# Optimization experiments

Hardware: AMD Instinct MI355X
Metric: run time of the kernel (lower is better)

The kernel has to match this reference:

```python
import jax, jax.numpy as jnp
import numpy as np

D = 128          # hidden_channels
NU = 50000       # num user nodes
NI = 50000       # num item nodes
E = 600000       # edges per edge type
SLOPE = 0.01     # F.leaky_relu default negative_slope


def setup_inputs() -> dict:
    key = jax.random.key(0)
    ks = jax.random.split(key, 24)
    ws = 1.0 / np.sqrt(D)  # xavier-ish scale

    def W2(i):  # stacked [n_layers=2, D, D] weight
        return jax.random.normal(ks[i], (2, D, D), jnp.float32) * ws

    def B2(i):  # stacked [2, D] bias
        return jax.random.normal(ks[i], (2, D), jnp.float32) * 0.01

    inp = {
        "x_user": jax.random.normal(ks[0], (NU, D), jnp.float32),
        "x_item": jax.random.normal(ks[1], (NI, D), jnp.float32),
        # row 0 = src indices, row 1 = dst indices
        "ei_ui": jax.random.randint(ks[2], (2, E), 0, NU),  # user -> item (dst in [0,NI))
        "ei_iu": jax.random.randint(ks[3], (2, E), 0, NI),  # item -> user (dst in [0,NU))
        # per-node-type q/k/v Linear params, stacked over the 2 layers
        "q_w_user": W2(4),  "q_b_user": B2(5),
        "k_w_user": W2(6),  "k_b_user": B2(7),
        "v_w_user": W2(8),  "v_b_user": B2(9),
        "q_w_item": W2(10), "q_b_item": B2(11),
        "k_w_item": W2(12), "k_b_item": B2(13),
        "v_w_item": W2(14), "v_b_item": B2(15),
        # per-edge-type bilinear W, stacked over the 2 layers
        "W_ui": W2(16),
        "W_iu": W2(17),
    }
    return inp


def _edge_agg(x_src, x_dst, qw, qb, kw, kb, vw, vb, W, src, dst, n_dst):
    # torch Linear: x @ w.T + b
    q = x_src @ qw.T + qb            # [Nsrc, D]
    k = x_dst @ kw.T + kb            # [Ndst, D]
    v = x_src @ vw.T + vb            # [Nsrc, D]
    qW = q @ W                       # project on nodes (cheaper than per-edge)
    # per-edge bilinear score q_src . W . k_dst / sqrt(D)
    score = jnp.sum(qW[src] * k[dst], axis=-1) * (1.0 / np.sqrt(D))  # [E]
    alpha = jax.nn.softmax(jax.nn.leaky_relu(score, SLOPE))          # softmax over edges
    msg = alpha[:, None] * v[src]                                    # [E, D]
    return jax.ops.segment_sum(msg, dst, num_segments=n_dst)


def _layer(x_u, x_i, ei_ui, ei_iu, p, l):
    # edge type (user, rates, item): q/v from src type (user), k from dst type (item)
    agg_i = _edge_agg(x_u, x_i,
                      p["q_w_user"][l], p["q_b_user"][l],
                      p["k_w_item"][l], p["k_b_item"][l],
                      p["v_w_user"][l], p["v_b_user"][l],
                      p["W_ui"][l], ei_ui[0], ei_ui[1], NI)
    # edge type (item, rev_rates, user)
    agg_u = _edge_agg(x_i, x_u,
                      p["q_w_item"][l], p["q_b_item"][l],
                      p["k_w_user"][l], p["k_b_user"][l],
                      p["v_w_item"][l], p["v_b_item"][l],
                      p["W_iu"][l], ei_iu[0], ei_iu[1], NU)
    # out_dict initialized with x_dst.clone(), then scatter_add
    return x_u + agg_u, x_i + agg_i


def reference(x_user, x_item, ei_ui, ei_iu,
              q_w_user, q_b_user, k_w_user, k_b_user, v_w_user, v_b_user,
              q_w_item, q_b_item, k_w_item, k_b_item, v_w_item, v_b_item,
              W_ui, W_iu):
    p = dict(q_w_user=q_w_user, q_b_user=q_b_user, k_w_user=k_w_user,
             k_b_user=k_b_user, v_w_user=v_w_user, v_b_user=v_b_user,
             q_w_item=q_w_item, q_b_item=q_b_item, k_w_item=k_w_item,
             k_b_item=k_b_item, v_w_item=v_w_item, v_b_item=v_b_item,
             W_ui=W_ui, W_iu=W_iu)
    x_u, x_i = _layer(x_user, x_item, ei_ui, ei_iu, p, 0)  # conv1
    x_u, x_i = _layer(x_u, x_i, ei_ui, ei_iu, p, 1)        # conv2
    return jnp.concatenate([x_u, x_i], axis=0)  # [NU+NI, D]
```

## Files before the change

kernel.cpp:

```cpp
#include <hip/hip_runtime.h>
#include <stdint.h>

#define D 128

typedef __attribute__((ext_vector_type(8))) short bf16x8;
typedef __attribute__((ext_vector_type(4))) float f32x4;
typedef __attribute__((ext_vector_type(2))) float f32x2;
typedef unsigned short u16;
typedef unsigned char u8;
typedef unsigned int u32;

#define KSCALE (0.08838834764831845f * 1.4426950408889634f)

#if defined(__has_builtin)
#if __has_builtin(__builtin_amdgcn_cvt_pk_f32_fp8) && __has_builtin(__builtin_amdgcn_cvt_pk_fp8_f32)
#define HW_FP8 1
#endif
#if __has_builtin(__builtin_elementwise_fma)
#define VFMA(a, b, c) __builtin_elementwise_fma(a, b, c)
#else
#define VFMA(a, b, c) ((a) * (b) + (c))
#endif
#else
#define VFMA(a, b, c) ((a) * (b) + (c))
#endif

static __device__ __forceinline__ float b2f(u16 u) {
  return __uint_as_float(((unsigned)u) << 16);
}
static __device__ __forceinline__ u16 f2b(float f) {
  unsigned u = __float_as_uint(f);
  return (u16)((u + 0x7fffu + ((u >> 16) & 1u)) >> 16);
}

static __device__ __forceinline__ u8 enc_fp8(float f) {
#ifdef HW_FP8
  int p = __builtin_amdgcn_cvt_pk_fp8_f32(f, 0.f, 0, false);
  return (u8)(p & 0xff);
#else
  float a = fabsf(f);
  unsigned s = (__float_as_uint(f) >> 31) << 7;
  if (a < 7.8125e-3f) {
    int m = (int)(a * 512.f + 0.5f);
    if (m > 7) m = 7;
    return (u8)(s | m);
  }
  int e; float mant = frexpf(a, &e);
  int E = e + 6;
  int m = (int)((2.f * mant - 1.f) * 8.f + 0.5f);
  if (m == 8) { m = 0; E++; }
  if (E > 15 || (E == 15 && m > 6)) { E = 15; m = 6; }
  if (E < 1) return (u8)s;
  return (u8)(s | (E << 3) | m);
#endif
}

static __device__ __forceinline__ float dec1_fp8(u8 b) {
  int e = (b >> 3) & 15, m = b & 7;
  float mag = e ? ldexpf((float)(8 + m), e - 10) : ldexpf((float)m, -9);
  return (b & 128) ? -mag : mag;
}

static __device__ __forceinline__ void dec8_fp8_v(u32 lo, u32 hi, f32x2* o) {
#ifdef HW_FP8
  o[0] = __builtin_amdgcn_cvt_pk_f32_fp8((int)lo, false);
  o[1] = __builtin_amdgcn_cvt_pk_f32_fp8((int)lo, true);
  o[2] = __builtin_amdgcn_cvt_pk_f32_fp8((int)hi, false);
  o[3] = __builtin_amdgcn_cvt_pk_f32_fp8((int)hi, true);
#else
  u32 w[2] = {lo, hi};
  u8* p = (u8*)w;
#pragma unroll
  for (int i = 0; i < 4; ++i) o[i] = (f32x2){dec1_fp8(p[2 * i]), dec1_fp8(p[2 * i + 1])};
#endif
}

template <int CTRL>
static __device__ __forceinline__ float dpp_add_f(float x) {
  int y = __builtin_amdgcn_update_dpp(0, __float_as_int(x), CTRL, 0xf, 0xf, true);
  return x + __int_as_float(y);
}

__global__ void prep_fused(const float* __restrict__ qwu, const float* __restrict__ qbu,
                           const float* __restrict__ qwi, const float* __restrict__ qbi,
                           const float* __restrict__ Wui, const float* __restrict__ Wiu,
                           u16* __restrict__ Mt, float* __restrict__ bq) {
  int c = blockIdx.y, d = blockIdx.x, j = threadIdx.x;
  int l = c & 1, type = c >> 1;
  const float* qw = (type ? qwi : qwu) + l * D * D;
  const float* qb = (type ? qbi : qbu) + l * D;
  const float* W  = (type ? Wiu : Wui) + l * D * D;
  float acc = 0.f;
  for (int cc = 0; cc < D; ++cc) acc += qw[cc * D + d] * W[cc * D + j];
  Mt[((size_t)c * D + j) * D + d] = f2b(acc);
  if (d == 0) {
    float ba = 0.f;
    for (int cc = 0; cc < D; ++cc) ba += qb[cc] * W[cc * D + j];
    bq[c * D + j] = ba;
  }
}

__global__ void cast_w(const float* __restrict__ kwu, const float* __restrict__ kwi,
                       const float* __restrict__ vwu, const float* __restrict__ vwi,
                       u16* __restrict__ Wb) {
  int y = blockIdx.y;
  const float* s = (y == 0) ? kwu : (y == 1) ? kwi : (y == 2) ? vwu : vwi;
  int i = blockIdx.x * 256 + threadIdx.x;
  Wb[(size_t)y * 2 * D * D + i] = f2b(s[i]);
}

__global__ void cast_x(const float* __restrict__ x, u16* __restrict__ xb, int n2) {
  int i = blockIdx.x * 256 + threadIdx.x;
  if (i < n2) {
    float2 v = ((const float2*)x)[i];
    ((unsigned*)xb)[i] = (unsigned)f2b(v.x) | ((unsigned)f2b(v.y) << 16);
  }
}

__global__ void zero_i(int* __restrict__ p, int n) {
  int i = blockIdx.x * 256 + threadIdx.x;
  if (i < n) p[i] = 0;
}

__global__ __launch_bounds__(256) void bhist(const int* __restrict__ dui,
                                             const int* __restrict__ diu,
                                             int* __restrict__ cnt_ui,
                                             int* __restrict__ cnt_iu, int E) {
  __shared__ int h[256];
  int t = threadIdx.x;
  h[t] = 0;
  __syncthreads();
  const int* dp = blockIdx.y ? diu : dui;
  int e0 = blockIdx.x * 1024;
#pragma unroll
  for (int i = 0; i < 4; ++i) {
    int e = e0 + i * 256 + t;
    if (e < E) atomicAdd(&h[dp[e] >> 8], 1);
  }
  __syncthreads();
  int* out = blockIdx.y ? cnt_iu : cnt_ui;
  if (h[t]) atomicAdd(&out[t], h[t]);
}

__global__ __launch_bounds__(256) void bscan(const int* __restrict__ cnt_ui,
                                             const int* __restrict__ cnt_iu,
                                             int* __restrict__ base_ui, int* __restrict__ base_iu,
                                             int* __restrict__ cur_ui, int* __restrict__ cur_iu,
                                             int* __restrict__ rp_ui, int* __restrict__ rp_iu,
                                             int nb_ui, int nb_iu, int n_ui, int n_iu, int E) {
  __shared__ int sh[256];
  int t = threadIdx.x;
  int v = (t < nb_ui) ? cnt_ui[t] : 0;
  sh[t] = v;
  __syncthreads();
  for (int off = 1; off < 256; off <<= 1) {
    int u = (t >= off) ? sh[t - off] : 0;
    __syncthreads();
    sh[t] += u;
    __syncthreads();
  }
  int ex = sh[t] - v;
  if (t < nb_ui) { base_ui[t] = ex; cur_ui[t] = ex; }
  if (t == 0) { base_ui[nb_ui] = E; rp_ui[n_ui] = E; }
  __syncthreads();
  v = (t < nb_iu) ? cnt_iu[t] : 0;
  sh[t] = v;
  __syncthreads();
  for (int off = 1; off < 256; off <<= 1) {
    int u = (t >= off) ? sh[t - off] : 0;
    __syncthreads();
    sh[t] += u;
    __syncthreads();
  }
  ex = sh[t] - v;
  if (t < nb_iu) { base_iu[t] = ex; cur_iu[t] = ex; }
  if (t == 0) { base_iu[nb_iu] = E; rp_iu[n_iu] = E; }
}

__global__ __launch_bounds__(256) void bscatter(
    const int* __restrict__ sui, const int* __restrict__ dui,
    const int* __restrict__ siu, const int* __restrict__ diu,
    int* __restrict__ cur_ui, int* __restrict__ cur_iu,
    u32* __restrict__ bb_ui, u32* __restrict__ bb_iu, int E) {
  __shared__ int h[256], rbase[256], c2[256];
  int t = threadIdx.x;
  const int* sp = blockIdx.y ? siu : sui;
  const int* dp = blockIdx.y ? diu : dui;
  int* gc = blockIdx.y ? cur_iu : cur_ui;
  u32* bb = blockIdx.y ? bb_iu : bb_ui;
  h[t] = 0;
  c2[t] = 0;
  __syncthreads();
  int e0 = blockIdx.x * 1024;
  u32 pr[4];
  int bk[4];
  bool act[4];
#pragma unroll
  for (int i = 0; i < 4; ++i) {
    int e = e0 + i * 256 + t;
    act[i] = e < E;
    if (act[i]) {
      int s = sp[e], d2 = dp[e];
      pr[i] = ((u32)d2 << 16) | (u32)s;
      bk[i] = d2 >> 8;
      atomicAdd(&h[bk[i]], 1);
    }
  }
  __syncthreads();
  if (h[t]) rbase[t] = atomicAdd(&gc[t], h[t]);
  __syncthreads();
#pragma unroll
  for (int i = 0; i < 4; ++i) {
    if (act[i]) {
      int r = atomicAdd(&c2[bk[i]], 1);
      bb[rbase[bk[i]] + r] = pr[i];
    }
  }
}

__global__ __launch_bounds__(256) void bsort(
    const u32* __restrict__ bb_ui, const u32* __restrict__ bb_iu,
    const int* __restrict__ base_ui, const int* __restrict__ base_iu,
    int* __restrict__ rp_ui, int* __restrict__ rp_iu,
    int* __restrict__ cs_ui, int* __restrict__ cs_iu,
    int nb_ui, int n_ui, int n_iu) {
  int b = blockIdx.x;
  const u32* bb; const int* base; int* rp; int* cs; int n;
  if (b < nb_ui) { bb = bb_ui; base = base_ui; rp = rp_ui; cs = cs_ui; n = n_ui; }
  else { b -= nb_ui; bb = bb_iu; base = base_iu; rp = rp_iu; cs = cs_iu; n = n_iu; }
  int lo = base[b], hi = base[b + 1];
  __shared__ int h[256], sh[256], cur[256];
  int t = threadIdx.x;
  h[t] = 0;
  __syncthreads();
  for (int j = lo + t; j < hi; j += 256) atomicAdd(&h[(bb[j] >> 16) & 255], 1);
  __syncthreads();
  int v = h[t];
  sh[t] = v;
  __syncthreads();
  for (int off = 1; off < 256; off <<= 1) {
    int u = (t >= off) ? sh[t - off] : 0;
    __syncthreads();
    sh[t] += u;
    __syncthreads();
  }
  int ex = lo + sh[t] - v;
  int gd = (b << 8) + t;
  if (gd < n) rp[gd] = ex;
  cur[t] = ex;
  __syncthreads();
  for (int j = lo + t; j < hi; j += 256) {
    u32 pr = bb[j];
    int p = atomicAdd(&cur[(pr >> 16) & 255], 1);
    cs[p] = (int)(pr & 0xffffu);
  }
}

__global__ __launch_bounds__(256) void gemm3(
    const u16* __restrict__ xu, const u16* __restrict__ xi,
    const u16* __restrict__ wqu, const u16* __restrict__ wku, const u16* __restrict__ wvu,
    const float* __restrict__ bqu, const float* __restrict__ bku, const float* __restrict__ bvu,
    const u16* __restrict__ wqi, const u16* __restrict__ wki, const u16* __restrict__ wvi,
    const float* __restrict__ bqi, const float* __restrict__ bki, const float* __restrict__ bvi,
    u8* __restrict__ Tqv_u, u16* __restrict__ Tk_u,
    u8* __restrict__ Tqv_i, u16* __restrict__ Tk_i,
    int gu, int nu, int ni) {
  __shared__ __align__(16) u16 wlds[128 * 136];
  int bx = blockIdx.x, y = blockIdx.y;
  bool item = bx >= gu;
  if (item) bx -= gu;
  const u16* x = item ? xi : xu;
  int nrows = item ? ni : nu;
  const u16* wt; const float* bias;
  if (y == 0)      { wt = item ? wqi : wqu; bias = item ? bqi : bqu; }
  else if (y == 1) { wt = item ? wki : wku; bias = item ? bki : bku; }
  else             { wt = item ? wvi : wvu; bias = item ? bvi : bvu; }
  u8* Tqv = item ? Tqv_i : Tqv_u;
  u16* Tk = item ? Tk_i : Tk_u;

  int t = threadIdx.x;
#pragma unroll
  for (int i = 0; i < 8; ++i) {
    int idx = t + 256 * i;
    int n = idx >> 4, kc = idx & 15;
    ((bf16x8*)wlds)[n * 17 + kc] = ((const bf16x8*)wt)[idx];
  }
  __syncthreads();
  int wave = t >> 6, lane = t & 63;
  int m = lane & 15, quad = lane >> 4;
  int row0 = bx * 64 + wave * 16;
  int arow = row0 + m;
  const bf16x8* xv = (const bf16x8*)(x + (size_t)(arow < nrows ? arow : 0) * D);
  f32x4 acc[8];
#pragma unroll
  for (int n = 0; n < 8; ++n) acc[n] = (f32x4){0.f, 0.f, 0.f, 0.f};
#pragma unroll
  for (int kk = 0; kk < 4; ++kk) {
    bf16x8 a = xv[kk * 4 + quad];
#pragma unroll
    for (int n = 0; n < 8; ++n) {
      bf16x8 b = ((const bf16x8*)wlds)[(n * 16 + m) * 17 + kk * 4 + quad];
      acc[n] = __builtin_amdgcn_mfma_f32_16x16x32_bf16(a, b, acc[n], 0, 0, 0);
    }
  }
  if (y == 1) {
#pragma unroll
    for (int n = 0; n < 8; ++n) {
      float bb = bias[n * 16 + m];
#pragma unroll
      for (int r = 0; r < 4; ++r) {
        int orow = row0 + quad * 4 + r;
        if (orow < nrows) Tk[(size_t)orow * D + n * 16 + m] = f2b((acc[n][r] + bb) * KSCALE);
      }
    }
  } else {
    int vo = (y == 0) ? 0 : 8;
#pragma unroll
    for (int n = 0; n < 8; ++n) {
      float bb = bias[n * 16 + m];
      int dim = n * 16 + m;
      int boff = ((dim >> 3) << 4) + (dim & 7) + vo;
#pragma unroll
      for (int r = 0; r < 4; ++r) {
        int orow = row0 + quad * 4 + r;
        if (orow < nrows) Tqv[(size_t)orow * 256 + boff] = enc_fp8(acc[n][r] + bb);
      }
    }
  }
}

static __device__ __forceinline__ void do_edge(uint4 w, bool act, const f32x2* kx,
                                               f32x2* acc, float& z) {
  f32x2 qx[4], vx[4];
  dec8_fp8_v(w.x, w.y, qx);
  dec8_fp8_v(w.z, w.w, vx);
  f32x2 d2 = qx[0] * kx[0];
  d2 = VFMA(qx[1], kx[1], d2);
  d2 = VFMA(qx[2], kx[2], d2);
  d2 = VFMA(qx[3], kx[3], d2);
  float dot = d2.x + d2.y;
  dot = dpp_add_f<0xB1>(dot);
  dot = dpp_add_f<0x4E>(dot);
  dot = dpp_add_f<0x128>(dot);
  dot = dpp_add_f<0x124>(dot);
  float sc = (dot > 0.f) ? dot : 0.01f * dot;
  float p = act ? exp2f(sc) : 0.f;
  z += p;
  f32x2 p2 = {p, p};
  acc[0] = VFMA(p2, vx[0], acc[0]);
  acc[1] = VFMA(p2, vx[1], acc[1]);
  acc[2] = VFMA(p2, vx[2], acc[2]);
  acc[3] = VFMA(p2, vx[3], acc[3]);
}

__global__ __launch_bounds__(256, 8) void agg_pass(
    const u8* __restrict__ Tqv_u, const u16* __restrict__ Tk_u,
    const u8* __restrict__ Tqv_i, const u16* __restrict__ Tk_i,
    const int* __restrict__ rp_ui, const int* __restrict__ cs_ui,
    const int* __restrict__ rp_iu, const int* __restrict__ cs_iu,
    float* __restrict__ agg_u, float* __restrict__ agg_i,
    float* __restrict__ zpart, int gai, int ni, int nu) {
  int bx = blockIdx.x;
  const u8* Pqv; const u16* Pk; const int* rp; const int* cs;
  float* agg; float* zp; int ndst;
  if (bx < gai) { Pqv = Tqv_u; Pk = Tk_i; rp = rp_ui; cs = cs_ui; agg = agg_i; zp = zpart; ndst = ni; }
  else { bx -= gai; Pqv = Tqv_i; Pk = Tk_u; rp = rp_iu; cs = cs_iu; agg = agg_u; zp = zpart + 1024; ndst = nu; }
  int wave = threadIdx.x >> 6, lane = threadIdx.x & 63;
  int d = bx * 4 + wave;
  int sub = lane & 15;
  int quad = lane >> 4;
  float z = 0.f;
  f32x2 acc[4] = {{0.f, 0.f}, {0.f, 0.f}, {0.f, 0.f}, {0.f, 0.f}};
  if (d < ndst) {
    bf16x8 kf = *(const bf16x8*)(Pk + (size_t)d * D + sub * 8);
    int beg = rp[d], end = rp[d + 1];
    f32x2 kx[4];
#pragma unroll
    for (int i = 0; i < 4; ++i)
      kx[i] = (f32x2){b2f((u16)((short*)&kf)[2 * i]), b2f((u16)((short*)&kf)[2 * i + 1])};
    const u8* Pq = Pqv + sub * 16;
    for (int j = beg; j < end; j += 16) {
      int rem = end - j;
      int e1 = end - 1;
      int i0 = j + quad, i1 = i0 + 4, i2 = i0 + 8, i3 = i0 + 12;
      int s0 = cs[i0 < end ? i0 : e1];
      int s1 = cs[i1 < end ? i1 : e1];
      int s2 = cs[i2 < end ? i2 : e1];
      int s3 = cs[i3 < end ? i3 : e1];
      uint4 w0 = *(const uint4*)(Pq + (size_t)s0 * 256);
      uint4 w1 = *(const uint4*)(Pq + (size_t)s1 * 256);
      uint4 w2 = *(const uint4*)(Pq + (size_t)s2 * 256);
      uint4 w3 = *(const uint4*)(Pq + (size_t)s3 * 256);
      do_edge(w0, i0 < end, kx, acc, z);
      if (rem > 4)  do_edge(w1, i1 < end, kx, acc, z);
      if (rem > 8)  do_edge(w2, i2 < end, kx, acc, z);
      if (rem > 12) do_edge(w3, i3 < end, kx, acc, z);
    }
    float* af = (float*)acc;
#pragma unroll
    for (int i = 0; i < 8; ++i) {
      af[i] += __shfl_xor(af[i], 16, 64);
      af[i] += __shfl_xor(af[i], 32, 64);
    }
    if (quad == 0) {
      float* ap = agg + (size_t)d * D + sub * 8;
      __builtin_nontemporal_store((f32x4){af[0], af[1], af[2], af[3]}, (f32x4*)ap);
      __builtin_nontemporal_store((f32x4){af[4], af[5], af[6], af[7]}, (f32x4*)ap + 1);
    }
    z += __shfl_xor(z, 16, 64);
    z += __shfl_xor(z, 32, 64);
  }
  __shared__ float ps[4];
  if (lane == 0) ps[wave] = z;
  __syncthreads();
  if (threadIdx.x == 0)
    unsafeAtomicAdd(&zp[blockIdx.x & 1023], ps[0] + ps[1] + ps[2] + ps[3]);
}

__global__ void zreduce(const float* __restrict__ zpart, float* __restrict__ zinv) {
  const float* zp = zpart + blockIdx.x * 1024;
  int t = threadIdx.x;
  float s = 0.f;
  for (int i = t; i < 1024; i += 256) s += zp[i];
  __shared__ float red[256];
  red[t] = s;
  __syncthreads();
  for (int k = 128; k > 0; k >>= 1) {
    if (t < k) red[t] += red[t + k];
    __syncthreads();
  }
  if (t == 0) zinv[blockIdx.x] = 1.0f / red[0];
}

__global__ void update_x(const float* __restrict__ xu, const float* __restrict__ xi,
                         const float* __restrict__ aggu, const float* __restrict__ aggi,
                         const float* __restrict__ zinv,
                         float* __restrict__ ou, float* __restrict__ oi,
                         u16* __restrict__ bu, u16* __restrict__ bi,
                         int nu4, int ni4, int wb) {
  int i = blockIdx.x * 256 + threadIdx.x;
  float zu = zinv[1];
  float zi = zinv[0];
  const float4* xs; const float4* as; float4* os; u16* bs; float zz; int jj;
  if (i < nu4) {
    xs = (const float4*)xu; as = (const float4*)aggu; os = (float4*)ou; bs = bu;
    zz = zu; jj = i;
  } else if (i < nu4 + ni4) {
    jj = i - nu4;
    xs = (const float4*)xi; as = (const float4*)aggi; os = (float4*)oi; bs = bi;
    zz = zi;
  } else {
    return;
  }
  float4 xv = xs[jj];
  float4 av = as[jj];
  float4 v;
  v.x = xv.x + av.x * zz;
  v.y = xv.y + av.y * zz;
  v.z = xv.z + av.z * zz;
  v.w = xv.w + av.w * zz;
  os[jj] = v;
  if (wb) {
    ushort4 b;
    b.x = f2b(v.x); b.y = f2b(v.y); b.z = f2b(v.z); b.w = f2b(v.w);
    ((ushort4*)bs)[jj] = b;
  }
}

extern "C" void kernel_launch(void* const* d_in, const int* in_sizes, int n_in,
                              void* d_out, int out_size, void* d_ws, size_t ws_size,
                              hipStream_t stream) {
  const float* xu_in = (const float*)d_in[0];
  const float* xi_in = (const float*)d_in[1];
  const int* ei_ui = (const int*)d_in[2];
  const int* ei_iu = (const int*)d_in[3];
  const float* qwu = (const float*)d_in[4];
  const float* qbu = (const float*)d_in[5];
  const float* kwu = (const float*)d_in[6];
  const float* kbu = (const float*)d_in[7];
  const float* vwu = (const float*)d_in[8];
  const float* vbu = (const float*)d_in[9];
  const float* qwi = (const float*)d_in[10];
  const float* qbi = (const float*)d_in[11];
  const float* kwi = (const float*)d_in[12];
  const float* kbi = (const float*)d_in[13];
  const float* vwi = (const float*)d_in[14];
  const float* vbi = (const float*)d_in[15];
  const float* Wui = (const float*)d_in[16];
  const float* Wiu = (const float*)d_in[17];

  int NU = in_sizes[0] / D;
  int NI = in_sizes[1] / D;
  int E  = in_sizes[2] / 2;

  char* w = (char*)d_ws;
  float* agg_u = (float*)w;  w += (size_t)NU * D * 4;
  float* agg_i = (float*)w;  w += (size_t)NI * D * 4;
  int* bcnt_ui = (int*)w;    w += 256 * 4;
  int* bcnt_iu = (int*)w;    w += 256 * 4;
  float* zpart = (float*)w;  w += 4096 * 4;
  float* zinv  = (float*)w;  w += 64;
  float* bq    = (float*)w;  w += 4 * D * 4;
  int* base_ui = (int*)w;    w += 260 * 4;
  int* base_iu = (int*)w;    w += 260 * 4;
  int* cur_ui  = (int*)w;    w += 256 * 4;
  int* cur_iu  = (int*)w;    w += 256 * 4;
  int* rp_ui = (int*)w;      w += (size_t)(NI + 4) * 4;
  int* rp_iu = (int*)w;      w += (size_t)(NU + 4) * 4;
  int* cs_ui = (int*)w;      w += (size_t)E * 4;
  int* cs_iu = (int*)w;      w += (size_t)E * 4;
  u32* bb_ui = (u32*)w;      w += (size_t)E * 4;
  u32* bb_iu = (u32*)w;      w += (size_t)E * 4;
  u16* Mt  = (u16*)w;        w += (size_t)4 * D * D * 2;
  u16* Wb  = (u16*)w;        w += (size_t)8 * D * D * 2;
  u16* xub = (u16*)w;        w += (size_t)NU * D * 2;
  u16* xib = (u16*)w;        w += (size_t)NI * D * 2;
  u16* Tk_u = (u16*)w;       w += (size_t)NU * D * 2;
  u16* Tk_i = (u16*)w;       w += (size_t)NI * D * 2;
  u8* Tqv_u = (u8*)w;        w += (size_t)NU * 256;
  u8* Tqv_i = (u8*)w;

  float* out_u = (float*)d_out;
  float* out_i = out_u + (size_t)NU * D;

  prep_fused<<<dim3(128, 4), 128, 0, stream>>>(qwu, qbu, qwi, qbi, Wui, Wiu, Mt, bq);
  cast_w<<<dim3(128, 4), 256, 0, stream>>>(kwu, kwi, vwu, vwi, Wb);
  cast_x<<<(NU * D / 2 + 255) / 256, 256, 0, stream>>>(xu_in, xub, NU * D / 2);
  cast_x<<<(NI * D / 2 + 255) / 256, 256, 0, stream>>>(xi_in, xib, NI * D / 2);

  int nb_ui = (NI + 255) >> 8;
  int nb_iu = (NU + 255) >> 8;
  zero_i<<<18, 256, 0, stream>>>(bcnt_ui, 512 + 4096);
  int geb = (E + 1023) / 1024;
  bhist<<<dim3(geb, 2), 256, 0, stream>>>(ei_ui + E, ei_iu + E, bcnt_ui, bcnt_iu, E);
  bscan<<<1, 256, 0, stream>>>(bcnt_ui, bcnt_iu, base_ui, base_iu, cur_ui, cur_iu,
                               rp_ui, rp_iu, nb_ui, nb_iu, NI, NU, E);
  bscatter<<<dim3(geb, 2), 256, 0, stream>>>(ei_ui, ei_ui + E, ei_iu, ei_iu + E,
                                             cur_ui, cur_iu, bb_ui, bb_iu, E);
  bsort<<<nb_ui + nb_iu, 256, 0, stream>>>(bb_ui, bb_iu, base_ui, base_iu,
                                           rp_ui, rp_iu, cs_ui, cs_iu, nb_ui, NI, NU);

  int gu = (NU + 63) / 64, gi = (NI + 63) / 64;
  int gau = (NU + 3) / 4, gai = (NI + 3) / 4;
  int nu4 = NU * D / 4, ni4 = NI * D / 4;
  int gup = (nu4 + ni4 + 255) / 256;

  for (int l = 0; l < 2; ++l) {
    gemm3<<<dim3(gu + gi, 3), 256, 0, stream>>>(
        xub, xib,
        Mt + (size_t)l * D * D, Wb + (size_t)(0 + l) * D * D, Wb + (size_t)(4 + l) * D * D,
        bq + l * D, kbu + l * D, vbu + l * D,
        Mt + (size_t)(2 + l) * D * D, Wb + (size_t)(2 + l) * D * D, Wb + (size_t)(6 + l) * D * D,
        bq + (2 + l) * D, kbi + l * D, vbi + l * D,
        Tqv_u, Tk_u, Tqv_i, Tk_i, gu, NU, NI);
    agg_pass<<<gai + gau, 256, 0, stream>>>(
        Tqv_u, Tk_u, Tqv_i, Tk_i, rp_ui, cs_ui, rp_iu, cs_iu,
        agg_u, agg_i, zpart + (size_t)l * 2 * 1024, gai, NI, NU);
    zreduce<<<2, 256, 0, stream>>>(zpart + (size_t)l * 2 * 1024, zinv + l * 2);
    if (l == 0)
      update_x<<<gup, 256, 0, stream>>>(xu_in, xi_in, agg_u, agg_i, zinv + l * 2,
                                        out_u, out_i, xub, xib, nu4, ni4, 1);
    else
      update_x<<<gup, 256, 0, stream>>>(out_u, out_i, agg_u, agg_i, zinv + l * 2,
                                        out_u, out_i, nullptr, nullptr, nu4, ni4, 0);
  }
}
```

Before: 469.6 us.

## Stage GEMM epilogue through LDS, split q/v fp8 layout, fold zreduce into update

The gemm3 epilogue now writes results into shared memory and then emits coalesced 16-byte row stores, instead of scattered 1- and 2-byte global stores. The fp8 q and v rows move from an interleaved layout to two contiguous 128-byte halves, so the edge kernel does two 8-byte gathers per edge instead of one 16-byte gather. The separate zreduce kernel is removed: every update_x block redundantly reduces the 2048 partial sums itself, which saves a launch but repeats the reduction in every block. Extra __syncthreads and LDS reuse are added to gemm3.

```diff
diff --git a/kernel.cpp b/kernel.cpp
--- a/kernel.cpp
+++ b/kernel.cpp
@@ -303,37 +303,54 @@
       acc[n] = __builtin_amdgcn_mfma_f32_16x16x32_bf16(a, b, acc[n], 0, 0, 0);
     }
   }
+  __syncthreads();
   if (y == 1) {
+    u16* ob = (u16*)wlds;
 #pragma unroll
     for (int n = 0; n < 8; ++n) {
       float bb = bias[n * 16 + m];
 #pragma unroll
       for (int r = 0; r < 4; ++r) {
-        int orow = row0 + quad * 4 + r;
-        if (orow < nrows) Tk[(size_t)orow * D + n * 16 + m] = f2b((acc[n][r] + bb) * KSCALE);
+        int rl = wave * 16 + quad * 4 + r;
+        ob[rl * 136 + n * 16 + m] = f2b((acc[n][r] + bb) * KSCALE);
       }
     }
+    __syncthreads();
+    int rl = t >> 2, c0 = (t & 3) * 32;
+    int orow = bx * 64 + rl;
+    if (orow < nrows) {
+      const uint4* src = (const uint4*)(ob + rl * 136 + c0);
+      uint4* dst = (uint4*)(Tk + (size_t)orow * 128 + c0);
+      dst[0] = src[0]; dst[1] = src[1]; dst[2] = src[2]; dst[3] = src[3];
+    }
   } else {
-    int vo = (y == 0) ? 0 : 8;
+    int vo = (y == 0) ? 0 : 128;
+    u8* ob = (u8*)wlds;
 #pragma unroll
     for (int n = 0; n < 8; ++n) {
       float bb = bias[n * 16 + m];
-      int dim = n * 16 + m;
-      int boff = ((dim >> 3) << 4) + (dim & 7) + vo;
 #pragma unroll
       for (int r = 0; r < 4; ++r) {
-        int orow = row0 + quad * 4 + r;
-        if (orow < nrows) Tqv[(size_t)orow * 256 + boff] = enc_fp8(acc[n][r] + bb);
+        int rl = wave * 16 + quad * 4 + r;
+        ob[rl * 144 + n * 16 + m] = enc_fp8(acc[n][r] + bb);
       }
     }
-  }
-}
-
-static __device__ __forceinline__ void do_edge(uint4 w, bool act, const f32x2* kx,
-                                               f32x2* acc, float& z) {
+    __syncthreads();
+    int rl = t >> 2, c0 = (t & 3) * 32;
+    int orow = bx * 64 + rl;
+    if (orow < nrows) {
+      const uint4* src = (const uint4*)(ob + rl * 144 + c0);
+      uint4* dst = (uint4*)(Tqv + (size_t)orow * 256 + vo + c0);
+      dst[0] = src[0]; dst[1] = src[1];
+    }
+  }
+}
+
+static __device__ __forceinline__ void do_edge(uint2 qw, uint2 vw, bool act,
+                                               const f32x2* kx, f32x2* acc, float& z) {
   f32x2 qx[4], vx[4];
-  dec8_fp8_v(w.x, w.y, qx);
-  dec8_fp8_v(w.z, w.w, vx);
+  dec8_fp8_v(qw.x, qw.y, qx);
+  dec8_fp8_v(vw.x, vw.y, vx);
   f32x2 d2 = qx[0] * kx[0];
   d2 = VFMA(qx[1], kx[1], d2);
   d2 = VFMA(qx[2], kx[2], d2);
@@ -378,7 +395,7 @@
 #pragma unroll
     for (int i = 0; i < 4; ++i)
       kx[i] = (f32x2){b2f((u16)((short*)&kf)[2 * i]), b2f((u16)((short*)&kf)[2 * i + 1])};
-    const u8* Pq = Pqv + sub * 16;
+    const u8* Pq = Pqv + sub * 8;
     for (int j = beg; j < end; j += 16) {
       int rem = end - j;
       int e1 = end - 1;
@@ -387,14 +404,22 @@
       int s1 = cs[i1 < end ? i1 : e1];
       int s2 = cs[i2 < end ? i2 : e1];
       int s3 = cs[i3 < end ? i3 : e1];
-      uint4 w0 = *(const uint4*)(Pq + (size_t)s0 * 256);
-      uint4 w1 = *(const uint4*)(Pq + (size_t)s1 * 256);
-      uint4 w2 = *(const uint4*)(Pq + (size_t)s2 * 256);
-      uint4 w3 = *(const uint4*)(Pq + (size_t)s3 * 256);
-      do_edge(w0, i0 < end, kx, acc, z);
-      if (rem > 4)  do_edge(w1, i1 < end, kx, acc, z);
-      if (rem > 8)  do_edge(w2, i2 < end, kx, acc, z);
-      if (rem > 12) do_edge(w3, i3 < end, kx, acc, z);
+      const u8* b0 = Pq + (size_t)s0 * 256;
+      const u8* b1 = Pq + (size_t)s1 * 256;
+      const u8* b2 = Pq + (size_t)s2 * 256;
+      const u8* b3 = Pq + (size_t)s3 * 256;
+      uint2 q0 = *(const uint2*)b0;
+      uint2 q1 = *(const uint2*)b1;
+      uint2 q2 = *(const uint2*)b2;
+      uint2 q3 = *(const uint2*)b3;
+      uint2 v0 = *(const uint2*)(b0 + 128);
+      uint2 v1 = *(const uint2*)(b1 + 128);
+      uint2 v2 = *(const uint2*)(b2 + 128);
+      uint2 v3 = *(const uint2*)(b3 + 128);
+      do_edge(q0, v0, i0 < end, kx, acc, z);
+      if (rem > 4)  do_edge(q1, v1, i1 < end, kx, acc, z);
+      if (rem > 8)  do_edge(q2, v2, i2 < end, kx, acc, z);
+      if (rem > 12) do_edge(q3, v3, i3 < end, kx, acc, z);
     }
     float* af = (float*)acc;
 #pragma unroll
@@ -417,30 +442,26 @@
     unsafeAtomicAdd(&zp[blockIdx.x & 1023], ps[0] + ps[1] + ps[2] + ps[3]);
 }
 
-__global__ void zreduce(const float* __restrict__ zpart, float* __restrict__ zinv) {
-  const float* zp = zpart + blockIdx.x * 1024;
-  int t = threadIdx.x;
-  float s = 0.f;
-  for (int i = t; i < 1024; i += 256) s += zp[i];
-  __shared__ float red[256];
-  red[t] = s;
-  __syncthreads();
-  for (int k = 128; k > 0; k >>= 1) {
-    if (t < k) red[t] += red[t + k];
-    __syncthreads();
-  }
-  if (t == 0) zinv[blockIdx.x] = 1.0f / red[0];
-}
-
 __global__ void update_x(const float* __restrict__ xu, const float* __restrict__ xi,
                          const float* __restrict__ aggu, const float* __restrict__ aggi,
-                         const float* __restrict__ zinv,
+                         const float* __restrict__ zpart,
                          float* __restrict__ ou, float* __restrict__ oi,
                          u16* __restrict__ bu, u16* __restrict__ bi,
                          int nu4, int ni4, int wb) {
-  int i = blockIdx.x * 256 + threadIdx.x;
-  float zu = zinv[1];
-  float zi = zinv[0];
+  __shared__ float red0[256], red1[256];
+  int t = threadIdx.x;
+  float s0 = zpart[t] + zpart[t + 256] + zpart[t + 512] + zpart[t + 768];
+  float s1 = zpart[1024 + t] + zpart[1280 + t] + zpart[1536 + t] + zpart[1792 + t];
+  red0[t] = s0;
+  red1[t] = s1;
+  __syncthreads();
+  for (int k = 128; k > 0; k >>= 1) {
+    if (t < k) { red0[t] += red0[t + k]; red1[t] += red1[t + k]; }
+    __syncthreads();
+  }
+  float zi = 1.0f / red0[0];
+  float zu = 1.0f / red1[0];
+  int i = blockIdx.x * 256 + t;
   const float4* xs; const float4* as; float4* os; u16* bs; float zz; int jj;
   if (i < nu4) {
     xs = (const float4*)xu; as = (const float4*)aggu; os = (float4*)ou; bs = bu;
@@ -499,7 +520,6 @@
   int* bcnt_ui = (int*)w;    w += 256 * 4;
   int* bcnt_iu = (int*)w;    w += 256 * 4;
   float* zpart = (float*)w;  w += 4096 * 4;
-  float* zinv  = (float*)w;  w += 64;
   float* bq    = (float*)w;  w += 4 * D * 4;
   int* base_ui = (int*)w;    w += 260 * 4;
   int* base_iu = (int*)w;    w += 260 * 4;
@@ -556,12 +576,13 @@
     agg_pass<<<gai + gau, 256, 0, stream>>>(
         Tqv_u, Tk_u, Tqv_i, Tk_i, rp_ui, cs_ui, rp_iu, cs_iu,
         agg_u, agg_i, zpart + (size_t)l * 2 * 1024, gai, NI, NU);
-    zreduce<<<2, 256, 0, stream>>>(zpart + (size_t)l * 2 * 1024, zinv + l * 2);
     if (l == 0)
-      update_x<<<gup, 256, 0, stream>>>(xu_in, xi_in, agg_u, agg_i, zinv + l * 2,
+      update_x<<<gup, 256, 0, stream>>>(xu_in, xi_in, agg_u, agg_i,
+                                        zpart + (size_t)l * 2 * 1024,
                                         out_u, out_i, xub, xib, nu4, ni4, 1);
     else
-      update_x<<<gup, 256, 0, stream>>>(out_u, out_i, agg_u, agg_i, zinv + l * 2,
+      update_x<<<gup, 256, 0, stream>>>(out_u, out_i, agg_u, agg_i,
+                                        zpart + (size_t)l * 2 * 1024,
                                         out_u, out_i, nullptr, nullptr, nu4, ni4, 0);
   }
 }
```

After: 462.0 us. About the same (-1.6%).
